# Kernel tuning notes

Measured on AMD Instinct MI355X. Metric: run time of the kernel, lower is better.

Reference implementation:

```python
import jax, jax.numpy as jnp
import numpy as np

HEADS = 16
DIM_HEAD = 64
SCALE = DIM_HEAD ** (-0.5)


def setup_inputs() -> dict:
    key = jax.random.key(0)
    ks = jax.random.split(key, 6)
    B, N, D = 2, 2048, 1024
    inner = HEADS * DIM_HEAD  # 1024
    s = 0.02
    return {
        "x": jax.random.normal(ks[0], (B, N, D), dtype=jnp.float32),
        "Wq": jax.random.normal(ks[1], (D, inner), dtype=jnp.float32) * s,
        "Wk": jax.random.normal(ks[2], (D, inner), dtype=jnp.float32) * s,
        "Wv": jax.random.normal(ks[3], (D, inner), dtype=jnp.float32) * s,
        "Wo": jax.random.normal(ks[4], (inner, D), dtype=jnp.float32) * s,
        "bo": jnp.zeros((D,), dtype=jnp.float32),
    }


def reference(x, Wq, Wk, Wv, Wo, bo):
    B, N, _ = x.shape
    # projections, split heads: [B, N, inner] -> [B, H, N, d]
    def split(t):
        return t.reshape(B, N, HEADS, DIM_HEAD).transpose(0, 2, 1, 3)
    q = split(x @ Wq)
    k = split(x @ Wk)  # self-attention: context = x
    v = split(x @ Wv)
    # scores [B, H, N, N], softmax over keys
    scores = jnp.einsum('bhid,bhjd->bhij', q, k) * SCALE
    attn = jax.nn.softmax(scores, axis=-1)
    out = jnp.einsum('bhij,bhjd->bhid', attn, v)
    out = out.transpose(0, 2, 1, 3).reshape(B, N, HEADS * DIM_HEAD)
    return out @ Wo + bo
```

## Files before the change

kernel.cpp:

```cpp
#include <hip/hip_runtime.h>
#include <hip/hip_bf16.h>
#include <stdint.h>

typedef unsigned short u16;
typedef __attribute__((ext_vector_type(8))) short bf16x8;
typedef __attribute__((ext_vector_type(4))) float f32x4;
typedef __attribute__((ext_vector_type(4))) unsigned int u32x4;

#define QSCALE 0.18033688011112042f

__device__ __forceinline__ u16 f2bf(float f) {
  return __builtin_bit_cast(u16, __float2bfloat16(f));
}

__device__ __forceinline__ uint32_t pkcvt(float a, float b) {
  return (uint32_t)f2bf(a) | ((uint32_t)f2bf(b) << 16);
}

__device__ __forceinline__ void gll16(const void* g, void* l) {
  __builtin_amdgcn_global_load_lds(
      (__attribute__((address_space(1))) void*)(uintptr_t)g,
      (__attribute__((address_space(3))) void*)l, 16, 0, 0);
}

__global__ __launch_bounds__(256)
void cvt_all_kernel(const float* __restrict__ x,
                    const float* __restrict__ Wq, const float* __restrict__ Wk,
                    const float* __restrict__ Wv, const float* __restrict__ Wo,
                    u16* __restrict__ xb, u16* __restrict__ Wqkvt, u16* __restrict__ Wot) {
  __shared__ float tile[32][33];
  const int bid = blockIdx.x, tid = threadIdx.x;
  if (bid < 4096) {
    const int z = bid >> 10, xy = bid & 1023;
    const float* src = (z == 0) ? Wq : (z == 1) ? Wk : (z == 2) ? Wv : Wo;
    const float scale = (z == 0) ? QSCALE : 1.0f;
    u16* dst = (z == 3) ? Wot : (Wqkvt + (size_t)z * 1024 * 1024);
    const int n0 = (xy & 31) * 32, k0 = (xy >> 5) * 32;
    const int tx = tid & 31, ty = tid >> 5;
#pragma unroll
    for (int i = 0; i < 4; ++i)
      tile[ty * 4 + i][tx] = src[(size_t)(k0 + ty * 4 + i) * 1024 + n0 + tx];
    __syncthreads();
#pragma unroll
    for (int i = 0; i < 4; ++i)
      dst[(size_t)(n0 + ty * 4 + i) * 1024 + k0 + tx] = f2bf(tile[tx][ty * 4 + i] * scale);
  } else {
    size_t i = (size_t)(bid - 4096) * 256 + tid;
    const float4* p = (const float4*)x + i * 2;
    float4 a = p[0], b = p[1];
    ushort4 lo, hi;
    lo.x = f2bf(a.x); lo.y = f2bf(a.y); lo.z = f2bf(a.z); lo.w = f2bf(a.w);
    hi.x = f2bf(b.x); hi.y = f2bf(b.y); hi.z = f2bf(b.z); hi.w = f2bf(b.w);
    ((ushort4*)xb)[i * 2]     = lo;
    ((ushort4*)xb)[i * 2 + 1] = hi;
  }
}

__global__ __launch_bounds__(256)
void gemm_qkv_kernel(const u16* __restrict__ A, const u16* __restrict__ Bt,
                     u16* __restrict__ Qb, u16* __restrict__ Kb, u16* __restrict__ Vtb) {
  __shared__ __align__(16) u16 As[128 * 32];
  __shared__ __align__(16) u16 Bs[128 * 32];
  const int row0 = blockIdx.x * 128, col0 = blockIdx.y * 128;
  const int tid = threadIdx.x, lane = tid & 63, wid = tid >> 6;
  const int wr = (wid >> 1) * 64, wc = (wid & 1) * 64;
  const int lr = lane & 15, lk = (lane >> 4) * 8;

  f32x4 acc[4][4];
#pragma unroll
  for (int m = 0; m < 4; ++m)
#pragma unroll
    for (int n = 0; n < 4; ++n) acc[m][n] = (f32x4){0.f, 0.f, 0.f, 0.f};

  const int c0 = wid * 128 + lane;

  for (int k0 = 0; k0 < 1024; k0 += 32) {
    __syncthreads();
#pragma unroll
    for (int c = 0; c < 2; ++c) {
      const int chunk = c0 + c * 64;
      const int r = chunk >> 2, kk = (chunk & 3) * 8;
      gll16(A + (size_t)(row0 + r) * 1024 + k0 + kk,
            (char*)As + (wid * 128 + c * 64) * 16);
      gll16(Bt + (size_t)(col0 + r) * 1024 + k0 + kk,
            (char*)Bs + (wid * 128 + c * 64) * 16);
    }
    __syncthreads();
    bf16x8 af[4], bfr[4];
#pragma unroll
    for (int m = 0; m < 4; ++m)
      af[m] = *(const bf16x8*)&As[(wr + m * 16 + lr) * 32 + lk];
#pragma unroll
    for (int n = 0; n < 4; ++n)
      bfr[n] = *(const bf16x8*)&Bs[(wc + n * 16 + lr) * 32 + lk];
#pragma unroll
    for (int m = 0; m < 4; ++m)
#pragma unroll
      for (int n = 0; n < 4; ++n)
        acc[m][n] = __builtin_amdgcn_mfma_f32_16x16x32_bf16(af[m], bfr[n], acc[m][n], 0, 0, 0);
  }

  const int lg = lane >> 4;
#pragma unroll
  for (int m = 0; m < 4; ++m) {
#pragma unroll
    for (int n = 0; n < 4; ++n) {
      const int gcol = col0 + wc + n * 16 + lr;
      const int w = gcol >> 10, rem = gcol & 1023;
      const int h = rem >> 6, dd = rem & 63;
      const int grow0 = row0 + wr + m * 16 + lg * 4;
      if (w == 2) {
        const int b0 = grow0 >> 11, nn0 = grow0 & 2047;
        const int kin = nn0 & 63;
        const int kp = (kin & 32) | ((kin & 12) << 1) | ((kin & 16) >> 2);
        ushort4 sv;
        sv.x = f2bf(acc[m][n][0]); sv.y = f2bf(acc[m][n][1]);
        sv.z = f2bf(acc[m][n][2]); sv.w = f2bf(acc[m][n][3]);
        *(ushort4*)&Vtb[((size_t)(b0 * 16 + h) * 64 + dd) * 2048 + (nn0 & ~63) + kp] = sv;
      } else {
#pragma unroll
        for (int r = 0; r < 4; ++r) {
          const int grow = grow0 + r;
          const int b = grow >> 11, nn = grow & 2047;
          const int bh = b * 16 + h;
          const u16 hv = f2bf(acc[m][n][r]);
          if (w == 0) Qb[((size_t)bh * 2048 + nn) * 64 + dd] = hv;
          else        Kb[((size_t)bh * 2048 + nn) * 64 + dd] = hv;
        }
      }
    }
  }
}

__global__ __launch_bounds__(256, 2)
void attn_kernel(const u16* __restrict__ Qb, const u16* __restrict__ Kb,
                 const u16* __restrict__ Vtb, u16* __restrict__ Ob) {
  __shared__ __align__(16) u16 Ks[2][64 * 64];
  __shared__ __align__(16) u16 Vs[2][64 * 64];
  const int tid = threadIdx.x, lane = tid & 63, wid = tid >> 6;
  const int bid = blockIdx.x;
  const int vv = (bid & 7) * 64 + (bid >> 3);
  const int qt = vv & 15, bh = vv >> 4;
  const int lr = lane & 15, lg = lane >> 4;

  const u16* Qp = Qb + ((size_t)bh * 2048 + qt * 128 + wid * 32) * 64;
  const char* Kg = (const char*)(Kb + (size_t)bh * 2048 * 64);
  const char* Vg = (const char*)(Vtb + (size_t)bh * 64 * 2048);

  bf16x8 aq[2][2];
#pragma unroll
  for (int qc = 0; qc < 2; ++qc)
#pragma unroll
    for (int ks = 0; ks < 2; ++ks)
      aq[qc][ks] = *(const bf16x8*)&Qp[(qc * 16 + lr) * 64 + ks * 32 + lg * 8];

  const int c_base = wid * 128 + lane;
  auto stage = [&](int buf, int kv0) {
#pragma unroll
    for (int i = 0; i < 2; ++i) {
      const int c = c_base + i * 64;
      const int row = c >> 3;
      const int sc = ((c & 7) * 16) ^ ((row & 7) << 4);
      gll16(Kg + (size_t)(kv0 + row) * 128 + sc, (char*)Ks[buf] + c * 16);
      gll16(Vg + (size_t)row * 4096 + kv0 * 2 + sc, (char*)Vs[buf] + c * 16);
    }
  };

  const int swz = (lr & 7) << 4;
  const int xk0 = (lg * 16) ^ swz;
  const int xk1 = (64 + lg * 16) ^ swz;

  f32x4 acco[4][2];
#pragma unroll
  for (int ct = 0; ct < 4; ++ct)
#pragma unroll
    for (int qc = 0; qc < 2; ++qc) acco[ct][qc] = (f32x4){0.f, 0.f, 0.f, 0.f};
  f32x4 lacc[2];
  lacc[0] = (f32x4){0.f, 0.f, 0.f, 0.f};
  lacc[1] = (f32x4){0.f, 0.f, 0.f, 0.f};
  const f32x4 minit = (f32x4){-8.f, -8.f, -8.f, -8.f};
  u32x4 ow;
  ow.x = ow.y = ow.z = ow.w = 0x3F803F80u;
  const bf16x8 ones = __builtin_bit_cast(bf16x8, ow);

  stage(0, 0);
  asm volatile("s_waitcnt vmcnt(0)" ::: "memory");
  __syncthreads();

  int buf = 0;
  for (int t = 0; t < 32; ++t) {
    if (t < 31) stage(buf ^ 1, (t + 1) * 64);
    const char* kbase = (const char*)Ks[buf] + lr * 128;
    const char* vbase = (const char*)Vs[buf] + lr * 128;

    bf16x8 kf[4][2];
#pragma unroll
    for (int kt = 0; kt < 4; ++kt) {
      kf[kt][0] = *(const bf16x8*)(kbase + kt * 2048 + xk0);
      kf[kt][1] = *(const bf16x8*)(kbase + kt * 2048 + xk1);
    }
    f32x4 s[4][2];
    __builtin_amdgcn_s_setprio(1);
#pragma unroll
    for (int kt = 0; kt < 4; ++kt)
#pragma unroll
      for (int qc = 0; qc < 2; ++qc) {
        f32x4 tacc = __builtin_amdgcn_mfma_f32_16x16x32_bf16(kf[kt][0], aq[qc][0], minit, 0, 0, 0);
        s[kt][qc]  = __builtin_amdgcn_mfma_f32_16x16x32_bf16(kf[kt][1], aq[qc][1], tacc, 0, 0, 0);
      }
    __builtin_amdgcn_s_setprio(0);
    bf16x8 pa[2][2];
#pragma unroll
    for (int qc = 0; qc < 2; ++qc) {
#pragma unroll
      for (int kt = 0; kt < 4; ++kt)
#pragma unroll
        for (int r = 0; r < 4; ++r)
          s[kt][qc][r] = __builtin_amdgcn_exp2f(s[kt][qc][r]);
#pragma unroll
      for (int ks = 0; ks < 2; ++ks) {
        u32x4 w;
        w.x = pkcvt(s[2 * ks][qc][0],     s[2 * ks][qc][1]);
        w.y = pkcvt(s[2 * ks][qc][2],     s[2 * ks][qc][3]);
        w.z = pkcvt(s[2 * ks + 1][qc][0], s[2 * ks + 1][qc][1]);
        w.w = pkcvt(s[2 * ks + 1][qc][2], s[2 * ks + 1][qc][3]);
        pa[qc][ks] = __builtin_bit_cast(bf16x8, w);
      }
      lacc[qc] = __builtin_amdgcn_mfma_f32_16x16x32_bf16(ones, pa[qc][0], lacc[qc], 0, 0, 0);
      lacc[qc] = __builtin_amdgcn_mfma_f32_16x16x32_bf16(ones, pa[qc][1], lacc[qc], 0, 0, 0);
    }
    __builtin_amdgcn_s_setprio(1);
#pragma unroll
    for (int ct = 0; ct < 4; ++ct) {
      const char* vb = vbase + ct * 2048;
#pragma unroll
      for (int ks = 0; ks < 2; ++ks) {
        bf16x8 vf = *(const bf16x8*)(vb + ((ks * 64 + lg * 16) ^ swz));
#pragma unroll
        for (int qc = 0; qc < 2; ++qc)
          acco[ct][qc] = __builtin_amdgcn_mfma_f32_16x16x32_bf16(vf, pa[qc][ks], acco[ct][qc], 0, 0, 0);
      }
    }
    __builtin_amdgcn_s_setprio(0);
    asm volatile("s_waitcnt vmcnt(0)" ::: "memory");
    __syncthreads();
    buf ^= 1;
  }

  const int b = bh >> 4, h = bh & 15;
#pragma unroll
  for (int qc = 0; qc < 2; ++qc) {
    const int q = qt * 128 + wid * 32 + qc * 16 + lr;
    const float inv = 1.0f / lacc[qc][0];
#pragma unroll
    for (int ct = 0; ct < 4; ++ct) {
      uint2 st;
      st.x = pkcvt(acco[ct][qc][0] * inv, acco[ct][qc][1] * inv);
      st.y = pkcvt(acco[ct][qc][2] * inv, acco[ct][qc][3] * inv);
      *(uint2*)&Ob[((size_t)b * 2048 + q) * 1024 + h * 64 + ct * 16 + lg * 4] = st;
    }
  }
}

__global__ __launch_bounds__(256)
void gemm_out_kernel(const u16* __restrict__ A, const u16* __restrict__ Bt,
                     const float* __restrict__ bo, float* __restrict__ out) {
  __shared__ __align__(16) u16 As[128 * 32];
  __shared__ __align__(16) u16 Bs[128 * 32];
  const int row0 = blockIdx.x * 128, col0 = blockIdx.y * 128;
  const int tid = threadIdx.x, lane = tid & 63, wid = tid >> 6;
  const int wr = (wid >> 1) * 64, wc = (wid & 1) * 64;
  const int lr = lane & 15, lk = (lane >> 4) * 8;

  f32x4 acc[4][4];
#pragma unroll
  for (int m = 0; m < 4; ++m)
#pragma unroll
    for (int n = 0; n < 4; ++n) acc[m][n] = (f32x4){0.f, 0.f, 0.f, 0.f};

  const int c0 = wid * 128 + lane;

  for (int k0 = 0; k0 < 1024; k0 += 32) {
    __syncthreads();
#pragma unroll
    for (int c = 0; c < 2; ++c) {
      const int chunk = c0 + c * 64;
      const int r = chunk >> 2, kk = (chunk & 3) * 8;
      gll16(A + (size_t)(row0 + r) * 1024 + k0 + kk,
            (char*)As + (wid * 128 + c * 64) * 16);
      gll16(Bt + (size_t)(col0 + r) * 1024 + k0 + kk,
            (char*)Bs + (wid * 128 + c * 64) * 16);
    }
    __syncthreads();
    bf16x8 af[4], bfr[4];
#pragma unroll
    for (int m = 0; m < 4; ++m)
      af[m] = *(const bf16x8*)&As[(wr + m * 16 + lr) * 32 + lk];
#pragma unroll
    for (int n = 0; n < 4; ++n)
      bfr[n] = *(const bf16x8*)&Bs[(wc + n * 16 + lr) * 32 + lk];
#pragma unroll
    for (int m = 0; m < 4; ++m)
#pragma unroll
      for (int n = 0; n < 4; ++n)
        acc[m][n] = __builtin_amdgcn_mfma_f32_16x16x32_bf16(af[m], bfr[n], acc[m][n], 0, 0, 0);
  }

  const int lg = lane >> 4;
#pragma unroll
  for (int m = 0; m < 4; ++m) {
#pragma unroll
    for (int n = 0; n < 4; ++n) {
      const int gcol = col0 + wc + n * 16 + lr;
      const float bv = bo[gcol];
#pragma unroll
      for (int r = 0; r < 4; ++r) {
        const int grow = row0 + wr + m * 16 + lg * 4 + r;
        out[(size_t)grow * 1024 + gcol] = acc[m][n][r] + bv;
      }
    }
  }
}

extern "C" void kernel_launch(void* const* d_in, const int* in_sizes, int n_in,
                              void* d_out, int out_size, void* d_ws, size_t ws_size,
                              hipStream_t stream) {
  const float* x  = (const float*)d_in[0];
  const float* Wq = (const float*)d_in[1];
  const float* Wk = (const float*)d_in[2];
  const float* Wv = (const float*)d_in[3];
  const float* Wo = (const float*)d_in[4];
  const float* bo = (const float*)d_in[5];
  float* out = (float*)d_out;

  char* ws = (char*)d_ws;
  u16* xb    = (u16*)(ws);
  u16* wqkvt = (u16*)(ws + ((size_t)8  << 20));
  u16* wot   = (u16*)(ws + ((size_t)14 << 20));
  u16* Qb    = (u16*)(ws + ((size_t)16 << 20));
  u16* Kb    = (u16*)(ws + ((size_t)24 << 20));
  u16* Vtb   = (u16*)(ws + ((size_t)32 << 20));
  u16* Ob    = xb;

  hipLaunchKernelGGL(cvt_all_kernel, dim3(6144), dim3(256), 0, stream,
                     x, Wq, Wk, Wv, Wo, xb, wqkvt, wot);
  hipLaunchKernelGGL(gemm_qkv_kernel, dim3(32, 24), dim3(256), 0, stream,
                     xb, wqkvt, Qb, Kb, Vtb);
  hipLaunchKernelGGL(attn_kernel, dim3(512), dim3(256), 0, stream,
                     Qb, Kb, Vtb, Ob);
  hipLaunchKernelGGL(gemm_out_kernel, dim3(32, 8), dim3(256), 0, stream,
                     Ob, wot, bo, out);
}
```

Before: 113.6 us.

## Double K-tile depth in GEMMs with swizzled LDS and widen attention KV tiles

Both projection GEMMs now stage 64-wide K slices instead of 32 per iteration. They use an XOR-swizzled LDS layout to avoid bank conflicts, which halves the number of barrier pairs per GEMM. The attention kernel stages 128 keys per double-buffered iteration, processed as two 64-key sub-blocks, which halves the barriers and waits. The cost is doubled LDS use (64 KB per attention block), which may limit occupancy under launch_bounds(256,2).

```diff
diff --git a/kernel.cpp b/kernel.cpp
--- a/kernel.cpp
+++ b/kernel.cpp
@@ -59,12 +59,13 @@
 __global__ __launch_bounds__(256)
 void gemm_qkv_kernel(const u16* __restrict__ A, const u16* __restrict__ Bt,
                      u16* __restrict__ Qb, u16* __restrict__ Kb, u16* __restrict__ Vtb) {
-  __shared__ __align__(16) u16 As[128 * 32];
-  __shared__ __align__(16) u16 Bs[128 * 32];
+  __shared__ __align__(16) u16 As[128 * 64];
+  __shared__ __align__(16) u16 Bs[128 * 64];
   const int row0 = blockIdx.x * 128, col0 = blockIdx.y * 128;
   const int tid = threadIdx.x, lane = tid & 63, wid = tid >> 6;
   const int wr = (wid >> 1) * 64, wc = (wid & 1) * 64;
-  const int lr = lane & 15, lk = (lane >> 4) * 8;
+  const int lr = lane & 15, lg = lane >> 4;
+  const int swz = (lr & 7) << 4;
 
   f32x4 acc[4][4];
 #pragma unroll
@@ -72,35 +73,36 @@
 #pragma unroll
     for (int n = 0; n < 4; ++n) acc[m][n] = (f32x4){0.f, 0.f, 0.f, 0.f};
 
-  const int c0 = wid * 128 + lane;
-
-  for (int k0 = 0; k0 < 1024; k0 += 32) {
-    __syncthreads();
-#pragma unroll
-    for (int c = 0; c < 2; ++c) {
-      const int chunk = c0 + c * 64;
-      const int r = chunk >> 2, kk = (chunk & 3) * 8;
-      gll16(A + (size_t)(row0 + r) * 1024 + k0 + kk,
-            (char*)As + (wid * 128 + c * 64) * 16);
-      gll16(Bt + (size_t)(col0 + r) * 1024 + k0 + kk,
-            (char*)Bs + (wid * 128 + c * 64) * 16);
-    }
-    __syncthreads();
-    bf16x8 af[4], bfr[4];
+  for (int k0 = 0; k0 < 1024; k0 += 64) {
+    __syncthreads();
+#pragma unroll
+    for (int i = 0; i < 4; ++i) {
+      const int c = tid + i * 256;
+      const int row = c >> 3;
+      const int sc = ((c & 7) * 16) ^ ((row & 7) << 4);
+      gll16((const char*)A  + ((size_t)(row0 + row) * 1024 + k0) * 2 + sc, (char*)As + c * 16);
+      gll16((const char*)Bt + ((size_t)(col0 + row) * 1024 + k0) * 2 + sc, (char*)Bs + c * 16);
+    }
+    __syncthreads();
+    bf16x8 af[4][2], bfr[4][2];
+#pragma unroll
+    for (int s = 0; s < 2; ++s) {
+#pragma unroll
+      for (int m = 0; m < 4; ++m)
+        af[m][s] = *(const bf16x8*)((const char*)As + (wr + m * 16 + lr) * 128 + ((s * 64 + lg * 16) ^ swz));
+#pragma unroll
+      for (int n = 0; n < 4; ++n)
+        bfr[n][s] = *(const bf16x8*)((const char*)Bs + (wc + n * 16 + lr) * 128 + ((s * 64 + lg * 16) ^ swz));
+    }
 #pragma unroll
     for (int m = 0; m < 4; ++m)
-      af[m] = *(const bf16x8*)&As[(wr + m * 16 + lr) * 32 + lk];
-#pragma unroll
-    for (int n = 0; n < 4; ++n)
-      bfr[n] = *(const bf16x8*)&Bs[(wc + n * 16 + lr) * 32 + lk];
-#pragma unroll
-    for (int m = 0; m < 4; ++m)
 #pragma unroll
       for (int n = 0; n < 4; ++n)
-        acc[m][n] = __builtin_amdgcn_mfma_f32_16x16x32_bf16(af[m], bfr[n], acc[m][n], 0, 0, 0);
-  }
-
-  const int lg = lane >> 4;
+#pragma unroll
+        for (int s = 0; s < 2; ++s)
+          acc[m][n] = __builtin_amdgcn_mfma_f32_16x16x32_bf16(af[m][s], bfr[n][s], acc[m][n], 0, 0, 0);
+  }
+
 #pragma unroll
   for (int m = 0; m < 4; ++m) {
 #pragma unroll
@@ -135,8 +137,8 @@
 __global__ __launch_bounds__(256, 2)
 void attn_kernel(const u16* __restrict__ Qb, const u16* __restrict__ Kb,
                  const u16* __restrict__ Vtb, u16* __restrict__ Ob) {
-  __shared__ __align__(16) u16 Ks[2][64 * 64];
-  __shared__ __align__(16) u16 Vs[2][64 * 64];
+  __shared__ __align__(16) u16 Ks[2][128 * 64];
+  __shared__ __align__(16) u16 Vs[2][128 * 64];
   const int tid = threadIdx.x, lane = tid & 63, wid = tid >> 6;
   const int bid = blockIdx.x;
   const int vv = (bid & 7) * 64 + (bid >> 3);
@@ -154,15 +156,15 @@
     for (int ks = 0; ks < 2; ++ks)
       aq[qc][ks] = *(const bf16x8*)&Qp[(qc * 16 + lr) * 64 + ks * 32 + lg * 8];
 
-  const int c_base = wid * 128 + lane;
   auto stage = [&](int buf, int kv0) {
 #pragma unroll
-    for (int i = 0; i < 2; ++i) {
-      const int c = c_base + i * 64;
+    for (int i = 0; i < 4; ++i) {
+      const int c = tid + i * 256;
       const int row = c >> 3;
       const int sc = ((c & 7) * 16) ^ ((row & 7) << 4);
       gll16(Kg + (size_t)(kv0 + row) * 128 + sc, (char*)Ks[buf] + c * 16);
-      gll16(Vg + (size_t)row * 4096 + kv0 * 2 + sc, (char*)Vs[buf] + c * 16);
+      gll16(Vg + (size_t)(row & 63) * 4096 + (size_t)(kv0 + (row >> 6) * 64) * 2 + sc,
+            (char*)Vs[buf] + c * 16);
     }
   };
 
@@ -188,60 +190,63 @@
   __syncthreads();
 
   int buf = 0;
-  for (int t = 0; t < 32; ++t) {
-    if (t < 31) stage(buf ^ 1, (t + 1) * 64);
-    const char* kbase = (const char*)Ks[buf] + lr * 128;
-    const char* vbase = (const char*)Vs[buf] + lr * 128;
-
-    bf16x8 kf[4][2];
-#pragma unroll
-    for (int kt = 0; kt < 4; ++kt) {
-      kf[kt][0] = *(const bf16x8*)(kbase + kt * 2048 + xk0);
-      kf[kt][1] = *(const bf16x8*)(kbase + kt * 2048 + xk1);
-    }
-    f32x4 s[4][2];
-    __builtin_amdgcn_s_setprio(1);
-#pragma unroll
-    for (int kt = 0; kt < 4; ++kt)
+  for (int t = 0; t < 16; ++t) {
+    if (t < 15) stage(buf ^ 1, (t + 1) * 128);
+#pragma unroll
+    for (int u = 0; u < 2; ++u) {
+      const char* kbase = (const char*)Ks[buf] + u * 8192 + lr * 128;
+      const char* vbase = (const char*)Vs[buf] + u * 8192 + lr * 128;
+
+      bf16x8 kf[4][2];
+#pragma unroll
+      for (int kt = 0; kt < 4; ++kt) {
+        kf[kt][0] = *(const bf16x8*)(kbase + kt * 2048 + xk0);
+        kf[kt][1] = *(const bf16x8*)(kbase + kt * 2048 + xk1);
+      }
+      f32x4 s[4][2];
+      __builtin_amdgcn_s_setprio(1);
+#pragma unroll
+      for (int kt = 0; kt < 4; ++kt)
+#pragma unroll
+        for (int qc = 0; qc < 2; ++qc) {
+          f32x4 tacc = __builtin_amdgcn_mfma_f32_16x16x32_bf16(kf[kt][0], aq[qc][0], minit, 0, 0, 0);
+          s[kt][qc]  = __builtin_amdgcn_mfma_f32_16x16x32_bf16(kf[kt][1], aq[qc][1], tacc, 0, 0, 0);
+        }
+      __builtin_amdgcn_s_setprio(0);
+      bf16x8 pa[2][2];
 #pragma unroll
       for (int qc = 0; qc < 2; ++qc) {
-        f32x4 tacc = __builtin_amdgcn_mfma_f32_16x16x32_bf16(kf[kt][0], aq[qc][0], minit, 0, 0, 0);
-        s[kt][qc]  = __builtin_amdgcn_mfma_f32_16x16x32_bf16(kf[kt][1], aq[qc][1], tacc, 0, 0, 0);
-      }
-    __builtin_amdgcn_s_setprio(0);
-    bf16x8 pa[2][2];
-#pragma unroll
-    for (int qc = 0; qc < 2; ++qc) {
-#pragma unroll
-      for (int kt = 0; kt < 4; ++kt)
-#pragma unroll
-        for (int r = 0; r < 4; ++r)
-          s[kt][qc][r] = __builtin_amdgcn_exp2f(s[kt][qc][r]);
-#pragma unroll
-      for (int ks = 0; ks < 2; ++ks) {
-        u32x4 w;
-        w.x = pkcvt(s[2 * ks][qc][0],     s[2 * ks][qc][1]);
-        w.y = pkcvt(s[2 * ks][qc][2],     s[2 * ks][qc][3]);
-        w.z = pkcvt(s[2 * ks + 1][qc][0], s[2 * ks + 1][qc][1]);
-        w.w = pkcvt(s[2 * ks + 1][qc][2], s[2 * ks + 1][qc][3]);
-        pa[qc][ks] = __builtin_bit_cast(bf16x8, w);
-      }
-      lacc[qc] = __builtin_amdgcn_mfma_f32_16x16x32_bf16(ones, pa[qc][0], lacc[qc], 0, 0, 0);
-      lacc[qc] = __builtin_amdgcn_mfma_f32_16x16x32_bf16(ones, pa[qc][1], lacc[qc], 0, 0, 0);
-    }
-    __builtin_amdgcn_s_setprio(1);
-#pragma unroll
-    for (int ct = 0; ct < 4; ++ct) {
-      const char* vb = vbase + ct * 2048;
-#pragma unroll
-      for (int ks = 0; ks < 2; ++ks) {
-        bf16x8 vf = *(const bf16x8*)(vb + ((ks * 64 + lg * 16) ^ swz));
-#pragma unroll
-        for (int qc = 0; qc < 2; ++qc)
-          acco[ct][qc] = __builtin_amdgcn_mfma_f32_16x16x32_bf16(vf, pa[qc][ks], acco[ct][qc], 0, 0, 0);
-      }
-    }
-    __builtin_amdgcn_s_setprio(0);
+#pragma unroll
+        for (int kt = 0; kt < 4; ++kt)
+#pragma unroll
+          for (int r = 0; r < 4; ++r)
+            s[kt][qc][r] = __builtin_amdgcn_exp2f(s[kt][qc][r]);
+#pragma unroll
+        for (int ks = 0; ks < 2; ++ks) {
+          u32x4 w;
+          w.x = pkcvt(s[2 * ks][qc][0],     s[2 * ks][qc][1]);
+          w.y = pkcvt(s[2 * ks][qc][2],     s[2 * ks][qc][3]);
+          w.z = pkcvt(s[2 * ks + 1][qc][0], s[2 * ks + 1][qc][1]);
+          w.w = pkcvt(s[2 * ks + 1][qc][2], s[2 * ks + 1][qc][3]);
+          pa[qc][ks] = __builtin_bit_cast(bf16x8, w);
+        }
+        lacc[qc] = __builtin_amdgcn_mfma_f32_16x16x32_bf16(ones, pa[qc][0], lacc[qc], 0, 0, 0);
+        lacc[qc] = __builtin_amdgcn_mfma_f32_16x16x32_bf16(ones, pa[qc][1], lacc[qc], 0, 0, 0);
+      }
+      __builtin_amdgcn_s_setprio(1);
+#pragma unroll
+      for (int ct = 0; ct < 4; ++ct) {
+        const char* vb = vbase + ct * 2048;
+#pragma unroll
+        for (int ks = 0; ks < 2; ++ks) {
+          bf16x8 vf = *(const bf16x8*)(vb + ((ks * 64 + lg * 16) ^ swz));
+#pragma unroll
+          for (int qc = 0; qc < 2; ++qc)
+            acco[ct][qc] = __builtin_amdgcn_mfma_f32_16x16x32_bf16(vf, pa[qc][ks], acco[ct][qc], 0, 0, 0);
+        }
+      }
+      __builtin_amdgcn_s_setprio(0);
+    }
     asm volatile("s_waitcnt vmcnt(0)" ::: "memory");
     __syncthreads();
     buf ^= 1;
@@ -265,12 +270,13 @@
 __global__ __launch_bounds__(256)
 void gemm_out_kernel(const u16* __restrict__ A, const u16* __restrict__ Bt,
                      const float* __restrict__ bo, float* __restrict__ out) {
-  __shared__ __align__(16) u16 As[128 * 32];
-  __shared__ __align__(16) u16 Bs[128 * 32];
+  __shared__ __align__(16) u16 As[128 * 64];
+  __shared__ __align__(16) u16 Bs[128 * 64];
   const int row0 = blockIdx.x * 128, col0 = blockIdx.y * 128;
   const int tid = threadIdx.x, lane = tid & 63, wid = tid >> 6;
   const int wr = (wid >> 1) * 64, wc = (wid & 1) * 64;
-  const int lr = lane & 15, lk = (lane >> 4) * 8;
+  const int lr = lane & 15, lg = lane >> 4;
+  const int swz = (lr & 7) << 4;
 
   f32x4 acc[4][4];
 #pragma unroll
@@ -278,35 +284,36 @@
 #pragma unroll
     for (int n = 0; n < 4; ++n) acc[m][n] = (f32x4){0.f, 0.f, 0.f, 0.f};
 
-  const int c0 = wid * 128 + lane;
-
-  for (int k0 = 0; k0 < 1024; k0 += 32) {
-    __syncthreads();
-#pragma unroll
-    for (int c = 0; c < 2; ++c) {
-      const int chunk = c0 + c * 64;
-      const int r = chunk >> 2, kk = (chunk & 3) * 8;
-      gll16(A + (size_t)(row0 + r) * 1024 + k0 + kk,
-            (char*)As + (wid * 128 + c * 64) * 16);
-      gll16(Bt + (size_t)(col0 + r) * 1024 + k0 + kk,
-            (char*)Bs + (wid * 128 + c * 64) * 16);
-    }
-    __syncthreads();
-    bf16x8 af[4], bfr[4];
+  for (int k0 = 0; k0 < 1024; k0 += 64) {
+    __syncthreads();
+#pragma unroll
+    for (int i = 0; i < 4; ++i) {
+      const int c = tid + i * 256;
+      const int row = c >> 3;
+      const int sc = ((c & 7) * 16) ^ ((row & 7) << 4);
+      gll16((const char*)A  + ((size_t)(row0 + row) * 1024 + k0) * 2 + sc, (char*)As + c * 16);
+      gll16((const char*)Bt + ((size_t)(col0 + row) * 1024 + k0) * 2 + sc, (char*)Bs + c * 16);
+    }
+    __syncthreads();
+    bf16x8 af[4][2], bfr[4][2];
+#pragma unroll
+    for (int s = 0; s < 2; ++s) {
+#pragma unroll
+      for (int m = 0; m < 4; ++m)
+        af[m][s] = *(const bf16x8*)((const char*)As + (wr + m * 16 + lr) * 128 + ((s * 64 + lg * 16) ^ swz));
+#pragma unroll
+      for (int n = 0; n < 4; ++n)
+        bfr[n][s] = *(const bf16x8*)((const char*)Bs + (wc + n * 16 + lr) * 128 + ((s * 64 + lg * 16) ^ swz));
+    }
 #pragma unroll
     for (int m = 0; m < 4; ++m)
-      af[m] = *(const bf16x8*)&As[(wr + m * 16 + lr) * 32 + lk];
-#pragma unroll
-    for (int n = 0; n < 4; ++n)
-      bfr[n] = *(const bf16x8*)&Bs[(wc + n * 16 + lr) * 32 + lk];
-#pragma unroll
-    for (int m = 0; m < 4; ++m)
 #pragma unroll
       for (int n = 0; n < 4; ++n)
-        acc[m][n] = __builtin_amdgcn_mfma_f32_16x16x32_bf16(af[m], bfr[n], acc[m][n], 0, 0, 0);
-  }
-
-  const int lg = lane >> 4;
+#pragma unroll
+        for (int s = 0; s < 2; ++s)
+          acc[m][n] = __builtin_amdgcn_mfma_f32_16x16x32_bf16(af[m][s], bfr[n][s], acc[m][n], 0, 0, 0);
+  }
+
 #pragma unroll
   for (int m = 0; m < 4; ++m) {
 #pragma unroll
```

New measurement: 119.8 us. +5.5%, slower.
